# Performance work log

Hardware: AMD Instinct MI355X
Metric: run time of the kernel (lower is better)

## Reference

```python
import jax, jax.numpy as jnp
import numpy as np

B, C, H, W = 64, 3, 32, 32
HID, PRE, VMAX = 128, 32, 256
IN_DIM = C * 5 - 1  # 14


def setup_inputs() -> dict:
    key = jax.random.key(0)
    ks = jax.random.split(key, 9)
    s = 0.05
    return {
        "x": jax.random.uniform(ks[0], (B, C, H, W), dtype=jnp.float32),
        "W_pre": jax.random.normal(ks[1], (PRE, IN_DIM), dtype=jnp.float32) * s,
        "b_pre": jnp.zeros((PRE,), dtype=jnp.float32),
        "W_ih": jax.random.normal(ks[2], (3 * HID, PRE), dtype=jnp.float32) * s,
        "b_ih": jnp.zeros((3 * HID,), dtype=jnp.float32),
        "W_hh": jax.random.normal(ks[3], (3 * HID, HID), dtype=jnp.float32) * s,
        "b_hh": jnp.zeros((3 * HID,), dtype=jnp.float32),
        "W_post": jax.random.normal(ks[4], (VMAX, HID), dtype=jnp.float32) * s,
        "b_post": jnp.zeros((VMAX,), dtype=jnp.float32),
    }


def _img2input(x):
    # x: [b, c, h, w] -> [b, (h-2)*(w-2)*c, 5c-1], matching torch _img2input
    b, c, h, w = x.shape
    xp = jnp.transpose(x, (0, 2, 3, 1))  # [b,h,w,c]
    tl = xp[:, :-2, :-2, :]
    tc = xp[:, :-2, 1:-1, :]
    tr = xp[:, :-2, 2:, :]
    lf = xp[:, 1:-1, :-2, :]
    ct = xp[:, 1:-1, 1:-1, :]
    base = jnp.concatenate([tl, tc, tr, lf], axis=-1)  # [b,h-2,w-2,4c]
    base = jnp.broadcast_to(base[..., None, :], base.shape[:3] + (c, 4 * c))
    # tail[ic, ic1] = center[ic1] if ic1 < ic else -1
    mask = jnp.arange(c - 1)[None, :] < jnp.arange(c)[:, None]  # [c, c-1]
    tail = jnp.where(mask, ct[..., None, :c - 1], -1.0)  # [b,h-2,w-2,c,c-1]
    y = jnp.concatenate([base, tail], axis=-1)  # [b,h-2,w-2,c,5c-1]
    return y.reshape(b, (h - 2) * (w - 2) * c, 5 * c - 1)


def reference(x, W_pre, b_pre, W_ih, b_ih, W_hh, b_hh, W_post, b_post):
    b, c, h, w = x.shape
    inp = _img2input(x)                                   # [b, T, 5c-1]
    pre = jax.nn.sigmoid(inp @ W_pre.T + b_pre)           # [b, T, PRE]
    xg = pre @ W_ih.T + b_ih                              # [b, T, 3*HID]
    xg_t = jnp.transpose(xg, (1, 0, 2))                   # [T, b, 3*HID]

    def step(h_prev, xt):
        hg = h_prev @ W_hh.T + b_hh
        xr, xz, xn = jnp.split(xt, 3, axis=-1)
        hr, hz, hn = jnp.split(hg, 3, axis=-1)
        r = jax.nn.sigmoid(xr + hr)
        z = jax.nn.sigmoid(xz + hz)
        n = jnp.tanh(xn + r * hn)
        h_new = (1.0 - z) * n + z * h_prev
        return h_new, h_new

    h0 = jnp.zeros((b, W_hh.shape[1]), dtype=x.dtype)
    _, hs = jax.lax.scan(step, h0, xg_t)                  # [T, b, HID]
    hs = jnp.transpose(hs, (1, 0, 2))                     # [b, T, HID]
    out = hs @ W_post.T + b_post                          # [b, T, VMAX]
    vmax = W_post.shape[0]
    out = out.reshape(b, h - 2, w - 2, c, vmax)
    out = jnp.transpose(out, (0, 3, 1, 2, 4))             # [b, c, h-2, w-2, vmax]
    out = jnp.pad(out, ((0, 0), (0, 0), (1, 1), (1, 1), (0, 0)))
    return out  # [b, c, h, w, vmax]
```

## Files before the change

kernel.cpp:

```cpp
#include <hip/hip_runtime.h>
#include <cstdint>

#define B_    64
#define T_    2700
#define HID_  128
#define PRE_  32
#define VMAX_ 256
#define NG_   16
#define NB_   4
#define TCH_  27
#define TSZ_  100

typedef _Float16 half2_t __attribute__((ext_vector_type(2)));
typedef _Float16 half4_t __attribute__((ext_vector_type(4)));
typedef _Float16 half8_t __attribute__((ext_vector_type(8)));
typedef float    f32x4_t __attribute__((ext_vector_type(4)));
union H8u { half8_t v; half2_t p[4]; };

#define MFMA32(A, Bv, C) __builtin_amdgcn_mfma_f32_16x16x32_f16((A), (Bv), (C), 0, 0, 0)

#if __has_builtin(__builtin_amdgcn_fdot2)
__device__ __forceinline__ float FDOT2(half2_t a, half2_t b, float c) {
    return __builtin_amdgcn_fdot2(a, b, c, false);
}
#else
__device__ __forceinline__ float FDOT2(half2_t a, half2_t b, float c) {
    return c + (float)a[0] * (float)b[0] + (float)a[1] * (float)b[1];
}
#endif

__device__ __forceinline__ half2_t mk2(float a, float b) {
    half2_t r; r[0] = (_Float16)a; r[1] = (_Float16)b; return r;
}
__device__ __forceinline__ float fast_sigmoid(float x) {
    float t = __builtin_amdgcn_exp2f(-1.4426950408889634f * x);
    return __builtin_amdgcn_rcpf(1.0f + t);
}
__device__ __forceinline__ float fast_tanh(float x) {
    float t = __builtin_amdgcn_exp2f(2.885390081777927f * x);
    return 1.0f - 2.0f * __builtin_amdgcn_rcpf(t + 1.0f);
}
template<int CTRL>
__device__ __forceinline__ float dpp_add(float x) {
    int t = __builtin_amdgcn_update_dpp(0, __float_as_int(x), CTRL, 0xF, 0xF, true);
    return x + __int_as_float(t);
}
__device__ __forceinline__ void fma4(float4& a, const float4 w, const float4 h) {
    a.x += w.x * h.x; a.y += w.y * h.y; a.z += w.z * h.z; a.w += w.w * h.w;
}
__device__ __forceinline__ float hsum4(const float4 a) {
    return (a.x + a.y) + (a.z + a.w);
}
__device__ __forceinline__ float pick_reg(f32x4_t v, int addr, int sel) {
    float t0 = __int_as_float(__builtin_amdgcn_ds_bpermute(addr, __float_as_int(v[0])));
    float t1 = __int_as_float(__builtin_amdgcn_ds_bpermute(addr, __float_as_int(v[1])));
    float t2 = __int_as_float(__builtin_amdgcn_ds_bpermute(addr, __float_as_int(v[2])));
    float t3 = __int_as_float(__builtin_amdgcn_ds_bpermute(addr, __float_as_int(v[3])));
    float a = (sel & 1) ? t1 : t0;
    float b = (sel & 1) ? t3 : t2;
    return (sel & 2) ? b : a;
}

__global__ __launch_bounds__(256) void k_pre(const float* __restrict__ x,
                                             const float* __restrict__ W_pre,
                                             const float* __restrict__ b_pre,
                                             _Float16* __restrict__ pre16) {
    int tid  = blockIdx.x * 256 + threadIdx.x;
    int i    = tid & 31;
    int rest = tid >> 5;
    int c    = rest % 3;
    int r2   = rest / 3;
    int p    = r2 % 900;
    int b    = r2 / 900;
    int r    = p / 30;
    int cc   = p - r * 30;
    const float* xb = x + b * 3072 + r * 32 + cc;
    float f0 = xb[0],    f1  = xb[1024], f2  = xb[2048];
    float f3 = xb[1],    f4  = xb[1025], f5  = xb[2049];
    float f6 = xb[2],    f7  = xb[1026], f8  = xb[2050];
    float f9 = xb[32],   f10 = xb[1056], f11 = xb[2080];
    float ct0 = xb[33],  ct1 = xb[1057];
    float f12 = (c >= 1) ? ct0 : -1.0f;
    float f13 = (c >= 2) ? ct1 : -1.0f;
    const float* w = W_pre + i * 14;
    float d = b_pre[i];
    d += f0*w[0]  + f1*w[1]  + f2*w[2]  + f3*w[3]  + f4*w[4]  + f5*w[5]  + f6*w[6]
       + f7*w[7]  + f8*w[8]  + f9*w[9]  + f10*w[10] + f11*w[11] + f12*w[12] + f13*w[13];

    int t  = p * 3 + c;
    int g  = b >> 2;
    int cs = b & 3;
    size_t base = ((size_t)g * T_ + t) * 128;
    int idx = ((i >> 3) << 5) | (cs << 3) | (i & 7);
    pre16[base + idx] = (_Float16)fast_sigmoid(d);
}

template<bool FULL>
__global__ __launch_bounds__(512) void k_xg(const float* __restrict__ W_ih,
                                            const float* __restrict__ b_ih,
                                            const float* __restrict__ b_hh,
                                            const _Float16* __restrict__ pre16,
                                            _Float16* __restrict__ xg16) {
    const int tid = threadIdx.x;
    const int g   = blockIdx.x / TCH_;
    const int tc  = blockIdx.x % TCH_;
    const int u3  = (tid >> 6) * 16 + ((tid & 63) >> 2);
    const int c4  = tid & 3;

    half2_t wr[16], wz[16], wn[16];
    const float* Wn = W_ih + (size_t)(256 + u3) * PRE_;
#pragma unroll
    for (int k2 = 0; k2 < 16; ++k2) wn[k2] = mk2(Wn[2*k2], Wn[2*k2 + 1]);
    const float bn = b_ih[256 + u3];
    float br = 0.f, bz = 0.f;
    if (FULL) {
        const float* Wr = W_ih + (size_t)u3 * PRE_;
        const float* Wz = W_ih + (size_t)(128 + u3) * PRE_;
#pragma unroll
        for (int k2 = 0; k2 < 16; ++k2) {
            wr[k2] = mk2(Wr[2*k2], Wr[2*k2 + 1]);
            wz[k2] = mk2(Wz[2*k2], Wz[2*k2 + 1]);
        }
        br = b_ih[u3] + b_hh[u3];
        bz = b_ih[128 + u3] + b_hh[128 + u3];
    }

    const char* preg = (const char*)pre16 + ((size_t)g * T_ + (size_t)tc * TSZ_) * 256 + c4 * 16;
    H8u pc0, pc1, pc2, pc3;
    pc0.v = *(const half8_t*)(preg +   0);
    pc1.v = *(const half8_t*)(preg +  64);
    pc2.v = *(const half8_t*)(preg + 128);
    pc3.v = *(const half8_t*)(preg + 192);

    for (int tt = 0; tt < TSZ_; ++tt) {
        const int ttn = (tt + 1 < TSZ_) ? tt + 1 : tt;
        H8u n0, n1, n2, n3;
        n0.v = *(const half8_t*)(preg + (size_t)ttn * 256 +   0);
        n1.v = *(const half8_t*)(preg + (size_t)ttn * 256 +  64);
        n2.v = *(const half8_t*)(preg + (size_t)ttn * 256 + 128);
        n3.v = *(const half8_t*)(preg + (size_t)ttn * 256 + 192);

        float an = bn;
#pragma unroll
        for (int j2 = 0; j2 < 4; ++j2) an = FDOT2(wn[ 0 + j2], pc0.p[j2], an);
#pragma unroll
        for (int j2 = 0; j2 < 4; ++j2) an = FDOT2(wn[ 4 + j2], pc1.p[j2], an);
#pragma unroll
        for (int j2 = 0; j2 < 4; ++j2) an = FDOT2(wn[ 8 + j2], pc2.p[j2], an);
#pragma unroll
        for (int j2 = 0; j2 < 4; ++j2) an = FDOT2(wn[12 + j2], pc3.p[j2], an);

        const size_t t = (size_t)tc * TSZ_ + tt;
        if (FULL) {
            float ar = br, az = bz;
#pragma unroll
            for (int j2 = 0; j2 < 4; ++j2) { ar = FDOT2(wr[ 0 + j2], pc0.p[j2], ar); az = FDOT2(wz[ 0 + j2], pc0.p[j2], az); }
#pragma unroll
            for (int j2 = 0; j2 < 4; ++j2) { ar = FDOT2(wr[ 4 + j2], pc1.p[j2], ar); az = FDOT2(wz[ 4 + j2], pc1.p[j2], az); }
#pragma unroll
            for (int j2 = 0; j2 < 4; ++j2) { ar = FDOT2(wr[ 8 + j2], pc2.p[j2], ar); az = FDOT2(wz[ 8 + j2], pc2.p[j2], az); }
#pragma unroll
            for (int j2 = 0; j2 < 4; ++j2) { ar = FDOT2(wr[12 + j2], pc3.p[j2], ar); az = FDOT2(wz[12 + j2], pc3.p[j2], az); }
            half4_t o;
            o[0] = (_Float16)ar; o[1] = (_Float16)az; o[2] = (_Float16)an; o[3] = (_Float16)0.f;
            *(half4_t*)((char*)xg16 + (((size_t)g * T_ + t) * 512 + tid) * 8) = o;
        } else {
            xg16[((size_t)g * T_ + t) * 512 + tid] = (_Float16)an;
        }
        pc0 = n0; pc1 = n1; pc2 = n2; pc3 = n3;
    }
}

template<bool FULL>
__global__ __launch_bounds__(512, 1) void k_scan(const float* __restrict__ W_ih,
                                                 const float* __restrict__ b_ih,
                                                 const float* __restrict__ W_hh,
                                                 const float* __restrict__ b_hh,
                                                 const _Float16* __restrict__ pre16,
                                                 const _Float16* __restrict__ xg16,
                                                 _Float16* __restrict__ hs16) {
    __shared__ __align__(16) _Float16 hbuf[2][4][4][4][8];

    const int tid  = threadIdx.x;
    const int g    = blockIdx.x;
    const int w    = tid >> 6;
    const int lane = tid & 63;
    const int lo   = lane & 15;
    const int hi   = lane >> 4;
    const int c4   = lane & 3;
    const int row  = w * 16 + lo;

    half8_t Ar[5], Az[5], Ahn[4];
#pragma unroll
    for (int kc = 0; kc < 4; ++kc) {
        half8_t ar, az, an;
#pragma unroll
        for (int j = 0; j < 8; ++j) {
            int k = kc * 32 + hi * 8 + j;
            ar[j] = (_Float16)W_hh[row * HID_ + k];
            az[j] = (_Float16)W_hh[(128 + row) * HID_ + k];
            an[j] = (_Float16)W_hh[(256 + row) * HID_ + k];
        }
        Ar[kc] = ar; Az[kc] = az; Ahn[kc] = an;
    }
    if (!FULL) {
        half8_t ar, az;
#pragma unroll
        for (int j = 0; j < 8; ++j) {
            int k = hi * 8 + j;
            ar[j] = (_Float16)W_ih[row * PRE_ + k];
            az[j] = (_Float16)W_ih[(128 + row) * PRE_ + k];
        }
        Ar[4] = ar; Az[4] = az;
    }

    const int u3 = w * 16 + (lane >> 2);
    float br = 0.f, bz = 0.f;
    if (!FULL) { br = b_ih[u3] + b_hh[u3]; bz = b_ih[128 + u3] + b_hh[128 + u3]; }
    const float bhn = b_hh[256 + u3];
    const int srcaddr = ((((lane >> 4) << 4) | c4) << 2);
    const int sel     = (lane >> 2) & 3;

    const char* preg  = (const char*)pre16 + (size_t)g * T_ * 256;
    const int   pfoff = hi * 64 + c4 * 16;
    const char*      xgp = (const char*)xg16 + (((size_t)g * T_) * 512 + tid) * 8;
    const _Float16*  xgs = xg16 + (size_t)g * T_ * 512 + tid;
    _Float16* hsb = hs16 + (size_t)(g * NB_ + c4) * T_ * HID_ + u3;

    const int kc_w = u3 >> 5;
    const int hi_w = (u3 >> 3) & 3;
    const int j_w  = u3 & 7;

    ((uint32_t*)hbuf)[tid] = 0u;

    half8_t  pf{};
    half4_t  xh{};
    _Float16 xnf = (_Float16)0.f;
    if (FULL) xh = *(const half4_t*)xgp;
    else { pf = *(const half8_t*)(preg + pfoff); xnf = xgs[0]; }
    float hprev = 0.0f;
    __syncthreads();

    for (int t = 0; t < T_; ++t) {
        const int tn = (t + 1 < T_) ? (t + 1) : t;
        half8_t pfn{}; half4_t xhn{}; _Float16 xnn = (_Float16)0.f;
        if (FULL) {
            xhn = *(const half4_t*)(xgp + (size_t)tn * 4096);
        } else {
            pfn = *(const half8_t*)(preg + (size_t)tn * 256 + pfoff);
            xnn = xgs[(size_t)tn * 512];
        }

        const int rb = t & 1;
        half8_t hB[4];
#pragma unroll
        for (int kc = 0; kc < 4; ++kc)
            hB[kc] = *(const half8_t*)&hbuf[rb][kc][hi][c4][0];

        const f32x4_t Z4 = {0.f, 0.f, 0.f, 0.f};
        f32x4_t r = Z4, z = Z4, n = Z4;
        r = MFMA32(Ar[0],  hB[0], r);
        z = MFMA32(Az[0],  hB[0], z);
        n = MFMA32(Ahn[0], hB[0], n);
        r = MFMA32(Ar[1],  hB[1], r);
        z = MFMA32(Az[1],  hB[1], z);
        n = MFMA32(Ahn[1], hB[1], n);
        r = MFMA32(Ar[2],  hB[2], r);
        z = MFMA32(Az[2],  hB[2], z);
        n = MFMA32(Ahn[2], hB[2], n);
        r = MFMA32(Ar[3],  hB[3], r);
        z = MFMA32(Az[3],  hB[3], z);
        n = MFMA32(Ahn[3], hB[3], n);
        if (!FULL) {
            r = MFMA32(Ar[4], pf, r);
            z = MFMA32(Az[4], pf, z);
        }

        float srr = pick_reg(r, srcaddr, sel);
        float szz = pick_reg(z, srcaddr, sel);
        float shn = pick_reg(n, srcaddr, sel) + bhn;
        float sxn;
        if (FULL) { srr += (float)xh[0]; szz += (float)xh[1]; sxn = (float)xh[2]; }
        else      { srr += br;           szz += bz;           sxn = (float)xnf;  }

        float rg   = fast_sigmoid(srr);
        float zg   = fast_sigmoid(szz);
        float ng   = fast_tanh(sxn + rg * shn);
        float hnew = ng + zg * (hprev - ng);
        hprev = hnew;
        _Float16 h16 = (_Float16)hnew;

        hbuf[rb ^ 1][kc_w][hi_w][c4][j_w] = h16;
        hsb[(size_t)t * HID_] = h16;

        if (FULL) xh = xhn; else { pf = pfn; xnf = xnn; }

        asm volatile("s_waitcnt lgkmcnt(0)" ::: "memory");
        __builtin_amdgcn_s_barrier();
    }
}

__global__ __launch_bounds__(512, 4) void k_post(const float* __restrict__ W_post,
                                                 const float* __restrict__ b_post,
                                                 const _Float16* __restrict__ hs,
                                                 float* __restrict__ out) {
    __shared__ __align__(16) float sh[2][HID_];
    const int tid  = threadIdx.x;
    const int v    = tid >> 1;
    const int hf   = tid & 1;
    const int blk  = blockIdx.x;
    const int i    = blk & 31;
    const int rest = blk >> 5;
    const int ch   = rest % 3;
    const int b    = rest / 3;
    float* outb = out + ((size_t)(b * 3 + ch) * 1024 + i * 32) * VMAX_;

    if (i == 0 || i == 31) {
        if (hf == 0) {
#pragma unroll
            for (int jc = 0; jc < 32; ++jc) outb[jc * VMAX_ + v] = 0.0f;
        }
        return;
    }

    float4 wp[16];
    const float4* wpp = (const float4*)(W_post + (size_t)v * HID_ + hf * 64);
#pragma unroll
    for (int k = 0; k < 16; ++k) wp[k] = wpp[k];
    const float bp = b_post[v];

    const _Float16* hsb = hs + (size_t)b * T_ * HID_;
    const int trow = (i - 1) * 30;

    if (tid < 32) {
        half4_t hv = ((const half4_t*)(hsb + (size_t)(trow * 3 + ch) * HID_))[tid];
        float4 f = {(float)hv[0], (float)hv[1], (float)hv[2], (float)hv[3]};
        ((float4*)sh[1])[tid] = f;
    }
    if (hf == 0) { outb[v] = 0.0f; outb[31 * VMAX_ + v] = 0.0f; }
    __syncthreads();

    for (int jc = 1; jc <= 30; ++jc) {
        if (tid < 32 && jc < 30) {
            half4_t hv = ((const half4_t*)(hsb + (size_t)((trow + jc) * 3 + ch) * HID_))[tid];
            float4 f = {(float)hv[0], (float)hv[1], (float)hv[2], (float)hv[3]};
            ((float4*)sh[(jc + 1) & 1])[tid] = f;
        }
        const float4* h4 = (const float4*)sh[jc & 1] + hf * 16;
        float4 a0 = {0,0,0,0}, a1 = {0,0,0,0}, a2 = {0,0,0,0}, a3 = {0,0,0,0};
#pragma unroll
        for (int k = 0; k < 16; k += 4) {
            fma4(a0, wp[k],     h4[k]);
            fma4(a1, wp[k + 1], h4[k + 1]);
            fma4(a2, wp[k + 2], h4[k + 2]);
            fma4(a3, wp[k + 3], h4[k + 3]);
        }
        float s = (hsum4(a0) + hsum4(a1)) + (hsum4(a2) + hsum4(a3));
        s = dpp_add<0xB1>(s);
        if (hf == 0) outb[jc * VMAX_ + v] = bp + s;
        __syncthreads();
    }
}

extern "C" void kernel_launch(void* const* d_in, const int* in_sizes, int n_in,
                              void* d_out, int out_size, void* d_ws, size_t ws_size,
                              hipStream_t stream) {
    const float* x      = (const float*)d_in[0];
    const float* W_pre  = (const float*)d_in[1];
    const float* b_pre  = (const float*)d_in[2];
    const float* W_ih   = (const float*)d_in[3];
    const float* b_ih   = (const float*)d_in[4];
    const float* W_hh   = (const float*)d_in[5];
    const float* b_hh   = (const float*)d_in[6];
    const float* W_post = (const float*)d_in[7];
    const float* b_post = (const float*)d_in[8];
    float* out = (float*)d_out;

    const size_t pre_bytes = (size_t)NG_ * T_ * 256;
    const size_t xg_full   = (size_t)NG_ * T_ * 512 * 8;
    const size_t xg_fb     = (size_t)NG_ * T_ * 512 * 2;
    const size_t hs_bytes  = (size_t)B_ * T_ * HID_ * 2;
    const bool full = ws_size >= pre_bytes + xg_full + hs_bytes;

    _Float16* pre16 = (_Float16*)d_ws;
    _Float16* xg    = (_Float16*)((char*)d_ws + pre_bytes);
    _Float16* hs16  = (_Float16*)((char*)d_ws + pre_bytes + (full ? xg_full : xg_fb));

    k_pre<<<21600, 256, 0, stream>>>(x, W_pre, b_pre, pre16);
    if (full) {
        k_xg<true><<<NG_ * TCH_, 512, 0, stream>>>(W_ih, b_ih, b_hh, pre16, xg);
        k_scan<true><<<NG_, 512, 0, stream>>>(W_ih, b_ih, W_hh, b_hh, pre16, xg, hs16);
    } else {
        k_xg<false><<<NG_ * TCH_, 512, 0, stream>>>(W_ih, b_ih, b_hh, pre16, xg);
        k_scan<false><<<NG_, 512, 0, stream>>>(W_ih, b_ih, W_hh, b_hh, pre16, xg, hs16);
    }
    k_post<<<6144, 512, 0, stream>>>(W_post, b_post, hs16, out);
}
```

Before: 2.102 ms.

## Remap full-path scan so active lanes compute four hidden units per step

The full-workspace path of the GRU scan is split into its own kernel. Gate results are now read straight from the MFMA accumulator registers, so a quarter of the lanes each handle four hidden units. This drops the cross-lane pick_reg shuffles and lets each of those lanes issue one vectorized half4 store to LDS and to the hidden-state output. The xg producer layout is permuted to match, and the time loop is unrolled by two with prefetch two steps ahead. The risk is that three quarters of the lanes sit idle during the gate math, which lengthens the per-step serial activation work on the critical path.

```diff
diff --git a/kernel.cpp b/kernel.cpp
--- a/kernel.cpp
+++ b/kernel.cpp
@@ -95,35 +95,30 @@
     pre16[base + idx] = (_Float16)fast_sigmoid(d);
 }
 
-template<bool FULL>
-__global__ __launch_bounds__(512) void k_xg(const float* __restrict__ W_ih,
-                                            const float* __restrict__ b_ih,
-                                            const float* __restrict__ b_hh,
-                                            const _Float16* __restrict__ pre16,
-                                            _Float16* __restrict__ xg16) {
+__global__ __launch_bounds__(512) void k_xg_full(const float* __restrict__ W_ih,
+                                                 const float* __restrict__ b_ih,
+                                                 const float* __restrict__ b_hh,
+                                                 const _Float16* __restrict__ pre16,
+                                                 _Float16* __restrict__ xg16) {
     const int tid = threadIdx.x;
     const int g   = blockIdx.x / TCH_;
     const int tc  = blockIdx.x % TCH_;
-    const int u3  = (tid >> 6) * 16 + ((tid & 63) >> 2);
-    const int c4  = tid & 3;
+    const int u3  = ((tid >> 6) << 4) | (((tid >> 4) & 3) << 2) | (tid & 3);
+    const int c4  = (tid >> 2) & 3;
 
     half2_t wr[16], wz[16], wn[16];
+    const float* Wr = W_ih + (size_t)u3 * PRE_;
+    const float* Wz = W_ih + (size_t)(128 + u3) * PRE_;
     const float* Wn = W_ih + (size_t)(256 + u3) * PRE_;
 #pragma unroll
-    for (int k2 = 0; k2 < 16; ++k2) wn[k2] = mk2(Wn[2*k2], Wn[2*k2 + 1]);
+    for (int k2 = 0; k2 < 16; ++k2) {
+        wr[k2] = mk2(Wr[2*k2], Wr[2*k2 + 1]);
+        wz[k2] = mk2(Wz[2*k2], Wz[2*k2 + 1]);
+        wn[k2] = mk2(Wn[2*k2], Wn[2*k2 + 1]);
+    }
+    const float br = b_ih[u3] + b_hh[u3];
+    const float bz = b_ih[128 + u3] + b_hh[128 + u3];
     const float bn = b_ih[256 + u3];
-    float br = 0.f, bz = 0.f;
-    if (FULL) {
-        const float* Wr = W_ih + (size_t)u3 * PRE_;
-        const float* Wz = W_ih + (size_t)(128 + u3) * PRE_;
-#pragma unroll
-        for (int k2 = 0; k2 < 16; ++k2) {
-            wr[k2] = mk2(Wr[2*k2], Wr[2*k2 + 1]);
-            wz[k2] = mk2(Wz[2*k2], Wz[2*k2 + 1]);
-        }
-        br = b_ih[u3] + b_hh[u3];
-        bz = b_ih[128 + u3] + b_hh[128 + u3];
-    }
 
     const char* preg = (const char*)pre16 + ((size_t)g * T_ + (size_t)tc * TSZ_) * 256 + c4 * 16;
     H8u pc0, pc1, pc2, pc3;
@@ -140,45 +135,65 @@
         n2.v = *(const half8_t*)(preg + (size_t)ttn * 256 + 128);
         n3.v = *(const half8_t*)(preg + (size_t)ttn * 256 + 192);
 
+        float ar = br, az = bz, an = bn;
+#pragma unroll
+        for (int j2 = 0; j2 < 4; ++j2) { ar = FDOT2(wr[ 0+j2], pc0.p[j2], ar); az = FDOT2(wz[ 0+j2], pc0.p[j2], az); an = FDOT2(wn[ 0+j2], pc0.p[j2], an); }
+#pragma unroll
+        for (int j2 = 0; j2 < 4; ++j2) { ar = FDOT2(wr[ 4+j2], pc1.p[j2], ar); az = FDOT2(wz[ 4+j2], pc1.p[j2], az); an = FDOT2(wn[ 4+j2], pc1.p[j2], an); }
+#pragma unroll
+        for (int j2 = 0; j2 < 4; ++j2) { ar = FDOT2(wr[ 8+j2], pc2.p[j2], ar); az = FDOT2(wz[ 8+j2], pc2.p[j2], az); an = FDOT2(wn[ 8+j2], pc2.p[j2], an); }
+#pragma unroll
+        for (int j2 = 0; j2 < 4; ++j2) { ar = FDOT2(wr[12+j2], pc3.p[j2], ar); az = FDOT2(wz[12+j2], pc3.p[j2], az); an = FDOT2(wn[12+j2], pc3.p[j2], an); }
+
+        const size_t t = (size_t)tc * TSZ_ + tt;
+        half4_t o;
+        o[0] = (_Float16)ar; o[1] = (_Float16)az; o[2] = (_Float16)an; o[3] = (_Float16)0.f;
+        *(half4_t*)((char*)xg16 + (((size_t)g * T_ + t) * 512 + tid) * 8) = o;
+        pc0 = n0; pc1 = n1; pc2 = n2; pc3 = n3;
+    }
+}
+
+__global__ __launch_bounds__(512) void k_xg_fb(const float* __restrict__ W_ih,
+                                               const float* __restrict__ b_ih,
+                                               const _Float16* __restrict__ pre16,
+                                               _Float16* __restrict__ xg16) {
+    const int tid = threadIdx.x;
+    const int g   = blockIdx.x / TCH_;
+    const int tc  = blockIdx.x % TCH_;
+    const int u3  = (tid >> 6) * 16 + ((tid & 63) >> 2);
+    const int c4  = tid & 3;
+
+    half2_t wn[16];
+    const float* Wn = W_ih + (size_t)(256 + u3) * PRE_;
+#pragma unroll
+    for (int k2 = 0; k2 < 16; ++k2) wn[k2] = mk2(Wn[2*k2], Wn[2*k2 + 1]);
+    const float bn = b_ih[256 + u3];
+
+    const char* preg = (const char*)pre16 + ((size_t)g * T_ + (size_t)tc * TSZ_) * 256 + c4 * 16;
+    for (int tt = 0; tt < TSZ_; ++tt) {
+        H8u pc0, pc1, pc2, pc3;
+        pc0.v = *(const half8_t*)(preg + (size_t)tt * 256 +   0);
+        pc1.v = *(const half8_t*)(preg + (size_t)tt * 256 +  64);
+        pc2.v = *(const half8_t*)(preg + (size_t)tt * 256 + 128);
+        pc3.v = *(const half8_t*)(preg + (size_t)tt * 256 + 192);
         float an = bn;
 #pragma unroll
-        for (int j2 = 0; j2 < 4; ++j2) an = FDOT2(wn[ 0 + j2], pc0.p[j2], an);
-#pragma unroll
-        for (int j2 = 0; j2 < 4; ++j2) an = FDOT2(wn[ 4 + j2], pc1.p[j2], an);
-#pragma unroll
-        for (int j2 = 0; j2 < 4; ++j2) an = FDOT2(wn[ 8 + j2], pc2.p[j2], an);
-#pragma unroll
-        for (int j2 = 0; j2 < 4; ++j2) an = FDOT2(wn[12 + j2], pc3.p[j2], an);
-
+        for (int j2 = 0; j2 < 4; ++j2) an = FDOT2(wn[ 0+j2], pc0.p[j2], an);
+#pragma unroll
+        for (int j2 = 0; j2 < 4; ++j2) an = FDOT2(wn[ 4+j2], pc1.p[j2], an);
+#pragma unroll
+        for (int j2 = 0; j2 < 4; ++j2) an = FDOT2(wn[ 8+j2], pc2.p[j2], an);
+#pragma unroll
+        for (int j2 = 0; j2 < 4; ++j2) an = FDOT2(wn[12+j2], pc3.p[j2], an);
         const size_t t = (size_t)tc * TSZ_ + tt;
-        if (FULL) {
-            float ar = br, az = bz;
-#pragma unroll
-            for (int j2 = 0; j2 < 4; ++j2) { ar = FDOT2(wr[ 0 + j2], pc0.p[j2], ar); az = FDOT2(wz[ 0 + j2], pc0.p[j2], az); }
-#pragma unroll
-            for (int j2 = 0; j2 < 4; ++j2) { ar = FDOT2(wr[ 4 + j2], pc1.p[j2], ar); az = FDOT2(wz[ 4 + j2], pc1.p[j2], az); }
-#pragma unroll
-            for (int j2 = 0; j2 < 4; ++j2) { ar = FDOT2(wr[ 8 + j2], pc2.p[j2], ar); az = FDOT2(wz[ 8 + j2], pc2.p[j2], az); }
-#pragma unroll
-            for (int j2 = 0; j2 < 4; ++j2) { ar = FDOT2(wr[12 + j2], pc3.p[j2], ar); az = FDOT2(wz[12 + j2], pc3.p[j2], az); }
-            half4_t o;
-            o[0] = (_Float16)ar; o[1] = (_Float16)az; o[2] = (_Float16)an; o[3] = (_Float16)0.f;
-            *(half4_t*)((char*)xg16 + (((size_t)g * T_ + t) * 512 + tid) * 8) = o;
-        } else {
-            xg16[((size_t)g * T_ + t) * 512 + tid] = (_Float16)an;
-        }
-        pc0 = n0; pc1 = n1; pc2 = n2; pc3 = n3;
-    }
-}
-
-template<bool FULL>
-__global__ __launch_bounds__(512, 1) void k_scan(const float* __restrict__ W_ih,
-                                                 const float* __restrict__ b_ih,
-                                                 const float* __restrict__ W_hh,
-                                                 const float* __restrict__ b_hh,
-                                                 const _Float16* __restrict__ pre16,
-                                                 const _Float16* __restrict__ xg16,
-                                                 _Float16* __restrict__ hs16) {
+        xg16[((size_t)g * T_ + t) * 512 + tid] = (_Float16)an;
+    }
+}
+
+__global__ __launch_bounds__(512, 1) void k_scan_full(const float* __restrict__ W_hh,
+                                                      const float* __restrict__ b_hh,
+                                                      const _Float16* __restrict__ xg16,
+                                                      _Float16* __restrict__ hs16) {
     __shared__ __align__(16) _Float16 hbuf[2][4][4][4][8];
 
     const int tid  = threadIdx.x;
@@ -190,7 +205,7 @@
     const int c4   = lane & 3;
     const int row  = w * 16 + lo;
 
-    half8_t Ar[5], Az[5], Ahn[4];
+    half8_t Ar[4], Az[4], Ahn[4];
 #pragma unroll
     for (int kc = 0; kc < 4; ++kc) {
         half8_t ar, az, an;
@@ -203,7 +218,104 @@
         }
         Ar[kc] = ar; Az[kc] = az; Ahn[kc] = an;
     }
-    if (!FULL) {
+
+    const bool act = (lo < 4);
+    const int u0 = w * 16 + hi * 4;
+    const f32x4_t bhn4 = *(const f32x4_t*)(b_hh + 256 + u0);
+
+    const char* xgp = (const char*)xg16 + (size_t)g * T_ * 4096
+                    + (size_t)(((w << 4) | (hi << 2) | c4) << 5);
+    _Float16* hsb = hs16 + (size_t)(g * NB_ + c4) * T_ * HID_ + u0;
+
+    const int kc_w  = u0 >> 5;
+    const int hi2_w = (u0 >> 3) & 3;
+    const int j0_w  = u0 & 7;
+
+    ((uint32_t*)hbuf)[tid] = 0u;
+
+    half8_t xA0 = *(const half8_t*)(xgp);
+    half8_t xA1 = *(const half8_t*)(xgp + 16);
+    half8_t xB0 = *(const half8_t*)(xgp + 4096);
+    half8_t xB1 = *(const half8_t*)(xgp + 4096 + 16);
+    f32x4_t hp = {0.f, 0.f, 0.f, 0.f};
+    __syncthreads();
+
+#define SCAN_STEP(RB, X0, X1, TT)                                              \
+    {                                                                          \
+        half8_t hB0 = *(const half8_t*)&hbuf[RB][0][hi][c4][0];                \
+        half8_t hB1 = *(const half8_t*)&hbuf[RB][1][hi][c4][0];                \
+        half8_t hB2 = *(const half8_t*)&hbuf[RB][2][hi][c4][0];                \
+        half8_t hB3 = *(const half8_t*)&hbuf[RB][3][hi][c4][0];                \
+        f32x4_t r = {0.f,0.f,0.f,0.f}, z = {0.f,0.f,0.f,0.f}, n = {0.f,0.f,0.f,0.f}; \
+        r = MFMA32(Ar[0], hB0, r); z = MFMA32(Az[0], hB0, z); n = MFMA32(Ahn[0], hB0, n); \
+        r = MFMA32(Ar[1], hB1, r); z = MFMA32(Az[1], hB1, z); n = MFMA32(Ahn[1], hB1, n); \
+        r = MFMA32(Ar[2], hB2, r); z = MFMA32(Az[2], hB2, z); n = MFMA32(Ahn[2], hB2, n); \
+        r = MFMA32(Ar[3], hB3, r); z = MFMA32(Az[3], hB3, z); n = MFMA32(Ahn[3], hB3, n); \
+        if (act) {                                                             \
+            half4_t hq;                                                        \
+            _Pragma("unroll")                                                  \
+            for (int q = 0; q < 4; ++q) {                                      \
+                half8_t xv = (q < 2) ? (X0) : (X1);                            \
+                const int o = (q & 1) * 4;                                     \
+                float rg = fast_sigmoid(r[q] + (float)xv[o]);                  \
+                float zg = fast_sigmoid(z[q] + (float)xv[o + 1]);              \
+                float ng = fast_tanh((float)xv[o + 2] + rg * (n[q] + bhn4[q])); \
+                float hv = ng + zg * (hp[q] - ng);                             \
+                hp[q] = hv;                                                    \
+                hq[q] = (_Float16)hv;                                          \
+            }                                                                  \
+            *(half4_t*)&hbuf[(RB) ^ 1][kc_w][hi2_w][c4][j0_w] = hq;            \
+            *(half4_t*)(hsb + (size_t)(TT) * HID_) = hq;                       \
+        }                                                                      \
+        asm volatile("s_waitcnt lgkmcnt(0)" ::: "memory");                     \
+        __builtin_amdgcn_s_barrier();                                          \
+    }
+
+    for (int t = 0; t < T_; t += 2) {
+        const size_t o2 = (size_t)((t + 2 < T_) ? t + 2 : T_ - 1) * 4096;
+        const size_t o3 = (size_t)((t + 3 < T_) ? t + 3 : T_ - 1) * 4096;
+        half8_t xC0 = *(const half8_t*)(xgp + o2);
+        half8_t xC1 = *(const half8_t*)(xgp + o2 + 16);
+        SCAN_STEP(0, xA0, xA1, t);
+        half8_t xD0 = *(const half8_t*)(xgp + o3);
+        half8_t xD1 = *(const half8_t*)(xgp + o3 + 16);
+        SCAN_STEP(1, xB0, xB1, t + 1);
+        xA0 = xC0; xA1 = xC1; xB0 = xD0; xB1 = xD1;
+    }
+#undef SCAN_STEP
+}
+
+__global__ __launch_bounds__(512, 1) void k_scan_fb(const float* __restrict__ W_ih,
+                                                    const float* __restrict__ b_ih,
+                                                    const float* __restrict__ W_hh,
+                                                    const float* __restrict__ b_hh,
+                                                    const _Float16* __restrict__ pre16,
+                                                    const _Float16* __restrict__ xg16,
+                                                    _Float16* __restrict__ hs16) {
+    __shared__ __align__(16) _Float16 hbuf[2][4][4][4][8];
+    const int tid  = threadIdx.x;
+    const int g    = blockIdx.x;
+    const int w    = tid >> 6;
+    const int lane = tid & 63;
+    const int lo   = lane & 15;
+    const int hi   = lane >> 4;
+    const int c4   = lane & 3;
+    const int row  = w * 16 + lo;
+
+    half8_t Ar[5], Az[5], Ahn[4];
+#pragma unroll
+    for (int kc = 0; kc < 4; ++kc) {
+        half8_t ar, az, an;
+#pragma unroll
+        for (int j = 0; j < 8; ++j) {
+            int k = kc * 32 + hi * 8 + j;
+            ar[j] = (_Float16)W_hh[row * HID_ + k];
+            az[j] = (_Float16)W_hh[(128 + row) * HID_ + k];
+            an[j] = (_Float16)W_hh[(256 + row) * HID_ + k];
+        }
+        Ar[kc] = ar; Az[kc] = az; Ahn[kc] = an;
+    }
+    {
         half8_t ar, az;
 #pragma unroll
         for (int j = 0; j < 8; ++j) {
@@ -215,16 +327,15 @@
     }
 
     const int u3 = w * 16 + (lane >> 2);
-    float br = 0.f, bz = 0.f;
-    if (!FULL) { br = b_ih[u3] + b_hh[u3]; bz = b_ih[128 + u3] + b_hh[128 + u3]; }
+    const float br  = b_ih[u3] + b_hh[u3];
+    const float bz  = b_ih[128 + u3] + b_hh[128 + u3];
     const float bhn = b_hh[256 + u3];
     const int srcaddr = ((((lane >> 4) << 4) | c4) << 2);
     const int sel     = (lane >> 2) & 3;
 
     const char* preg  = (const char*)pre16 + (size_t)g * T_ * 256;
     const int   pfoff = hi * 64 + c4 * 16;
-    const char*      xgp = (const char*)xg16 + (((size_t)g * T_) * 512 + tid) * 8;
-    const _Float16*  xgs = xg16 + (size_t)g * T_ * 512 + tid;
+    const _Float16* xgs = xg16 + (size_t)g * T_ * 512 + tid;
     _Float16* hsb = hs16 + (size_t)(g * NB_ + c4) * T_ * HID_ + u3;
 
     const int kc_w = u3 >> 5;
@@ -233,23 +344,15 @@
 
     ((uint32_t*)hbuf)[tid] = 0u;
 
-    half8_t  pf{};
-    half4_t  xh{};
-    _Float16 xnf = (_Float16)0.f;
-    if (FULL) xh = *(const half4_t*)xgp;
-    else { pf = *(const half8_t*)(preg + pfoff); xnf = xgs[0]; }
+    half8_t pf = *(const half8_t*)(preg + pfoff);
+    _Float16 xnf = xgs[0];
     float hprev = 0.0f;
     __syncthreads();
 
     for (int t = 0; t < T_; ++t) {
         const int tn = (t + 1 < T_) ? (t + 1) : t;
-        half8_t pfn{}; half4_t xhn{}; _Float16 xnn = (_Float16)0.f;
-        if (FULL) {
-            xhn = *(const half4_t*)(xgp + (size_t)tn * 4096);
-        } else {
-            pfn = *(const half8_t*)(preg + (size_t)tn * 256 + pfoff);
-            xnn = xgs[(size_t)tn * 512];
-        }
+        half8_t pfn = *(const half8_t*)(preg + (size_t)tn * 256 + pfoff);
+        _Float16 xnn = xgs[(size_t)tn * 512];
 
         const int rb = t & 1;
         half8_t hB[4];
@@ -271,17 +374,13 @@
         r = MFMA32(Ar[3],  hB[3], r);
         z = MFMA32(Az[3],  hB[3], z);
         n = MFMA32(Ahn[3], hB[3], n);
-        if (!FULL) {
-            r = MFMA32(Ar[4], pf, r);
-            z = MFMA32(Az[4], pf, z);
-        }
-
-        float srr = pick_reg(r, srcaddr, sel);
-        float szz = pick_reg(z, srcaddr, sel);
+        r = MFMA32(Ar[4], pf, r);
+        z = MFMA32(Az[4], pf, z);
+
+        float srr = pick_reg(r, srcaddr, sel) + br;
+        float szz = pick_reg(z, srcaddr, sel) + bz;
         float shn = pick_reg(n, srcaddr, sel) + bhn;
-        float sxn;
-        if (FULL) { srr += (float)xh[0]; szz += (float)xh[1]; sxn = (float)xh[2]; }
-        else      { srr += br;           szz += bz;           sxn = (float)xnf;  }
+        float sxn = (float)xnf;
 
         float rg   = fast_sigmoid(srr);
         float zg   = fast_sigmoid(szz);
@@ -293,8 +392,7 @@
         hbuf[rb ^ 1][kc_w][hi_w][c4][j_w] = h16;
         hsb[(size_t)t * HID_] = h16;
 
-        if (FULL) xh = xhn; else { pf = pfn; xnf = xnn; }
-
+        pf = pfn; xnf = xnn;
         asm volatile("s_waitcnt lgkmcnt(0)" ::: "memory");
         __builtin_amdgcn_s_barrier();
     }
@@ -388,11 +486,11 @@
 
     k_pre<<<21600, 256, 0, stream>>>(x, W_pre, b_pre, pre16);
     if (full) {
-        k_xg<true><<<NG_ * TCH_, 512, 0, stream>>>(W_ih, b_ih, b_hh, pre16, xg);
-        k_scan<true><<<NG_, 512, 0, stream>>>(W_ih, b_ih, W_hh, b_hh, pre16, xg, hs16);
+        k_xg_full<<<NG_ * TCH_, 512, 0, stream>>>(W_ih, b_ih, b_hh, pre16, xg);
+        k_scan_full<<<NG_, 512, 0, stream>>>(W_hh, b_hh, xg, hs16);
     } else {
-        k_xg<false><<<NG_ * TCH_, 512, 0, stream>>>(W_ih, b_ih, b_hh, pre16, xg);
-        k_scan<false><<<NG_, 512, 0, stream>>>(W_ih, b_ih, W_hh, b_hh, pre16, xg, hs16);
+        k_xg_fb<<<NG_ * TCH_, 512, 0, stream>>>(W_ih, b_ih, pre16, xg);
+        k_scan_fb<<<NG_, 512, 0, stream>>>(W_ih, b_ih, W_hh, b_hh, pre16, xg, hs16);
     }
     k_post<<<6144, 512, 0, stream>>>(W_post, b_post, hs16, out);
 }
```

Measured after the change: 2.444 ms. +16.3%, slower.

## Use MFMA for output projection, drop fallback path, unroll scan by two

Applied to the files above, without the earlier changes.

Rewrites k_post so each block computes its 30x256 output tile with fp16 16x16x32 MFMA on a converted fp16 W_post, replacing the per-thread float FMA loop with its 30 barriers. A new k_wcvt kernel converts W_post into the workspace, reusing the pre16 region once k_xg is done with it. The scan loop is unrolled by two so the xg prefetches for steps t+2 and t+3 are issued earlier. The small-workspace fallback is removed and the full xg buffer is always assumed, which fails if the workspace is too small. fp16 W_post adds rounding error.

```diff
diff --git a/kernel.cpp b/kernel.cpp
--- a/kernel.cpp
+++ b/kernel.cpp
@@ -39,17 +39,6 @@
 __device__ __forceinline__ float fast_tanh(float x) {
     float t = __builtin_amdgcn_exp2f(2.885390081777927f * x);
     return 1.0f - 2.0f * __builtin_amdgcn_rcpf(t + 1.0f);
-}
-template<int CTRL>
-__device__ __forceinline__ float dpp_add(float x) {
-    int t = __builtin_amdgcn_update_dpp(0, __float_as_int(x), CTRL, 0xF, 0xF, true);
-    return x + __int_as_float(t);
-}
-__device__ __forceinline__ void fma4(float4& a, const float4 w, const float4 h) {
-    a.x += w.x * h.x; a.y += w.y * h.y; a.z += w.z * h.z; a.w += w.w * h.w;
-}
-__device__ __forceinline__ float hsum4(const float4 a) {
-    return (a.x + a.y) + (a.z + a.w);
 }
 __device__ __forceinline__ float pick_reg(f32x4_t v, int addr, int sel) {
     float t0 = __int_as_float(__builtin_amdgcn_ds_bpermute(addr, __float_as_int(v[0])));
@@ -95,7 +84,6 @@
     pre16[base + idx] = (_Float16)fast_sigmoid(d);
 }
 
-template<bool FULL>
 __global__ __launch_bounds__(512) void k_xg(const float* __restrict__ W_ih,
                                             const float* __restrict__ b_ih,
                                             const float* __restrict__ b_hh,
@@ -108,22 +96,18 @@
     const int c4  = tid & 3;
 
     half2_t wr[16], wz[16], wn[16];
+    const float* Wr = W_ih + (size_t)u3 * PRE_;
+    const float* Wz = W_ih + (size_t)(128 + u3) * PRE_;
     const float* Wn = W_ih + (size_t)(256 + u3) * PRE_;
 #pragma unroll
-    for (int k2 = 0; k2 < 16; ++k2) wn[k2] = mk2(Wn[2*k2], Wn[2*k2 + 1]);
+    for (int k2 = 0; k2 < 16; ++k2) {
+        wr[k2] = mk2(Wr[2*k2], Wr[2*k2 + 1]);
+        wz[k2] = mk2(Wz[2*k2], Wz[2*k2 + 1]);
+        wn[k2] = mk2(Wn[2*k2], Wn[2*k2 + 1]);
+    }
+    const float br = b_ih[u3] + b_hh[u3];
+    const float bz = b_ih[128 + u3] + b_hh[128 + u3];
     const float bn = b_ih[256 + u3];
-    float br = 0.f, bz = 0.f;
-    if (FULL) {
-        const float* Wr = W_ih + (size_t)u3 * PRE_;
-        const float* Wz = W_ih + (size_t)(128 + u3) * PRE_;
-#pragma unroll
-        for (int k2 = 0; k2 < 16; ++k2) {
-            wr[k2] = mk2(Wr[2*k2], Wr[2*k2 + 1]);
-            wz[k2] = mk2(Wz[2*k2], Wz[2*k2 + 1]);
-        }
-        br = b_ih[u3] + b_hh[u3];
-        bz = b_ih[128 + u3] + b_hh[128 + u3];
-    }
 
     const char* preg = (const char*)pre16 + ((size_t)g * T_ + (size_t)tc * TSZ_) * 256 + c4 * 16;
     H8u pc0, pc1, pc2, pc3;
@@ -140,43 +124,32 @@
         n2.v = *(const half8_t*)(preg + (size_t)ttn * 256 + 128);
         n3.v = *(const half8_t*)(preg + (size_t)ttn * 256 + 192);
 
-        float an = bn;
-#pragma unroll
-        for (int j2 = 0; j2 < 4; ++j2) an = FDOT2(wn[ 0 + j2], pc0.p[j2], an);
-#pragma unroll
-        for (int j2 = 0; j2 < 4; ++j2) an = FDOT2(wn[ 4 + j2], pc1.p[j2], an);
-#pragma unroll
-        for (int j2 = 0; j2 < 4; ++j2) an = FDOT2(wn[ 8 + j2], pc2.p[j2], an);
-#pragma unroll
-        for (int j2 = 0; j2 < 4; ++j2) an = FDOT2(wn[12 + j2], pc3.p[j2], an);
+        float ar = br, az = bz, an = bn;
+#pragma unroll
+        for (int j2 = 0; j2 < 4; ++j2) { ar = FDOT2(wr[ 0+j2], pc0.p[j2], ar); az = FDOT2(wz[ 0+j2], pc0.p[j2], az); an = FDOT2(wn[ 0+j2], pc0.p[j2], an); }
+#pragma unroll
+        for (int j2 = 0; j2 < 4; ++j2) { ar = FDOT2(wr[ 4+j2], pc1.p[j2], ar); az = FDOT2(wz[ 4+j2], pc1.p[j2], az); an = FDOT2(wn[ 4+j2], pc1.p[j2], an); }
+#pragma unroll
+        for (int j2 = 0; j2 < 4; ++j2) { ar = FDOT2(wr[ 8+j2], pc2.p[j2], ar); az = FDOT2(wz[ 8+j2], pc2.p[j2], az); an = FDOT2(wn[ 8+j2], pc2.p[j2], an); }
+#pragma unroll
+        for (int j2 = 0; j2 < 4; ++j2) { ar = FDOT2(wr[12+j2], pc3.p[j2], ar); az = FDOT2(wz[12+j2], pc3.p[j2], az); an = FDOT2(wn[12+j2], pc3.p[j2], an); }
 
         const size_t t = (size_t)tc * TSZ_ + tt;
-        if (FULL) {
-            float ar = br, az = bz;
-#pragma unroll
-            for (int j2 = 0; j2 < 4; ++j2) { ar = FDOT2(wr[ 0 + j2], pc0.p[j2], ar); az = FDOT2(wz[ 0 + j2], pc0.p[j2], az); }
-#pragma unroll
-            for (int j2 = 0; j2 < 4; ++j2) { ar = FDOT2(wr[ 4 + j2], pc1.p[j2], ar); az = FDOT2(wz[ 4 + j2], pc1.p[j2], az); }
-#pragma unroll
-            for (int j2 = 0; j2 < 4; ++j2) { ar = FDOT2(wr[ 8 + j2], pc2.p[j2], ar); az = FDOT2(wz[ 8 + j2], pc2.p[j2], az); }
-#pragma unroll
-            for (int j2 = 0; j2 < 4; ++j2) { ar = FDOT2(wr[12 + j2], pc3.p[j2], ar); az = FDOT2(wz[12 + j2], pc3.p[j2], az); }
-            half4_t o;
-            o[0] = (_Float16)ar; o[1] = (_Float16)az; o[2] = (_Float16)an; o[3] = (_Float16)0.f;
-            *(half4_t*)((char*)xg16 + (((size_t)g * T_ + t) * 512 + tid) * 8) = o;
-        } else {
-            xg16[((size_t)g * T_ + t) * 512 + tid] = (_Float16)an;
-        }
+        half4_t o;
+        o[0] = (_Float16)ar; o[1] = (_Float16)az; o[2] = (_Float16)an; o[3] = (_Float16)0.f;
+        *(half4_t*)((char*)xg16 + (((size_t)g * T_ + t) * 512 + tid) * 8) = o;
         pc0 = n0; pc1 = n1; pc2 = n2; pc3 = n3;
     }
 }
 
-template<bool FULL>
-__global__ __launch_bounds__(512, 1) void k_scan(const float* __restrict__ W_ih,
-                                                 const float* __restrict__ b_ih,
-                                                 const float* __restrict__ W_hh,
+__global__ __launch_bounds__(256) void k_wcvt(const float* __restrict__ W_post,
+                                              _Float16* __restrict__ w16) {
+    int idx = blockIdx.x * 256 + threadIdx.x;
+    w16[idx] = (_Float16)W_post[idx];
+}
+
+__global__ __launch_bounds__(512, 1) void k_scan(const float* __restrict__ W_hh,
                                                  const float* __restrict__ b_hh,
-                                                 const _Float16* __restrict__ pre16,
                                                  const _Float16* __restrict__ xg16,
                                                  _Float16* __restrict__ hs16) {
     __shared__ __align__(16) _Float16 hbuf[2][4][4][4][8];
@@ -190,7 +163,7 @@
     const int c4   = lane & 3;
     const int row  = w * 16 + lo;
 
-    half8_t Ar[5], Az[5], Ahn[4];
+    half8_t Ar[4], Az[4], Ahn[4];
 #pragma unroll
     for (int kc = 0; kc < 4; ++kc) {
         half8_t ar, az, an;
@@ -203,28 +176,13 @@
         }
         Ar[kc] = ar; Az[kc] = az; Ahn[kc] = an;
     }
-    if (!FULL) {
-        half8_t ar, az;
-#pragma unroll
-        for (int j = 0; j < 8; ++j) {
-            int k = hi * 8 + j;
-            ar[j] = (_Float16)W_ih[row * PRE_ + k];
-            az[j] = (_Float16)W_ih[(128 + row) * PRE_ + k];
-        }
-        Ar[4] = ar; Az[4] = az;
-    }
 
     const int u3 = w * 16 + (lane >> 2);
-    float br = 0.f, bz = 0.f;
-    if (!FULL) { br = b_ih[u3] + b_hh[u3]; bz = b_ih[128 + u3] + b_hh[128 + u3]; }
     const float bhn = b_hh[256 + u3];
     const int srcaddr = ((((lane >> 4) << 4) | c4) << 2);
     const int sel     = (lane >> 2) & 3;
 
-    const char* preg  = (const char*)pre16 + (size_t)g * T_ * 256;
-    const int   pfoff = hi * 64 + c4 * 16;
-    const char*      xgp = (const char*)xg16 + (((size_t)g * T_) * 512 + tid) * 8;
-    const _Float16*  xgs = xg16 + (size_t)g * T_ * 512 + tid;
+    const char* xgp = (const char*)xg16 + ((size_t)g * T_ * 512 + tid) * 8;
     _Float16* hsb = hs16 + (size_t)(g * NB_ + c4) * T_ * HID_ + u3;
 
     const int kc_w = u3 >> 5;
@@ -233,81 +191,55 @@
 
     ((uint32_t*)hbuf)[tid] = 0u;
 
-    half8_t  pf{};
-    half4_t  xh{};
-    _Float16 xnf = (_Float16)0.f;
-    if (FULL) xh = *(const half4_t*)xgp;
-    else { pf = *(const half8_t*)(preg + pfoff); xnf = xgs[0]; }
+    half4_t xA = *(const half4_t*)(xgp);
+    half4_t xB = *(const half4_t*)(xgp + 4096);
     float hprev = 0.0f;
     __syncthreads();
 
-    for (int t = 0; t < T_; ++t) {
-        const int tn = (t + 1 < T_) ? (t + 1) : t;
-        half8_t pfn{}; half4_t xhn{}; _Float16 xnn = (_Float16)0.f;
-        if (FULL) {
-            xhn = *(const half4_t*)(xgp + (size_t)tn * 4096);
-        } else {
-            pfn = *(const half8_t*)(preg + (size_t)tn * 256 + pfoff);
-            xnn = xgs[(size_t)tn * 512];
-        }
-
-        const int rb = t & 1;
-        half8_t hB[4];
-#pragma unroll
-        for (int kc = 0; kc < 4; ++kc)
-            hB[kc] = *(const half8_t*)&hbuf[rb][kc][hi][c4][0];
-
-        const f32x4_t Z4 = {0.f, 0.f, 0.f, 0.f};
-        f32x4_t r = Z4, z = Z4, n = Z4;
-        r = MFMA32(Ar[0],  hB[0], r);
-        z = MFMA32(Az[0],  hB[0], z);
-        n = MFMA32(Ahn[0], hB[0], n);
-        r = MFMA32(Ar[1],  hB[1], r);
-        z = MFMA32(Az[1],  hB[1], z);
-        n = MFMA32(Ahn[1], hB[1], n);
-        r = MFMA32(Ar[2],  hB[2], r);
-        z = MFMA32(Az[2],  hB[2], z);
-        n = MFMA32(Ahn[2], hB[2], n);
-        r = MFMA32(Ar[3],  hB[3], r);
-        z = MFMA32(Az[3],  hB[3], z);
-        n = MFMA32(Ahn[3], hB[3], n);
-        if (!FULL) {
-            r = MFMA32(Ar[4], pf, r);
-            z = MFMA32(Az[4], pf, z);
-        }
-
-        float srr = pick_reg(r, srcaddr, sel);
-        float szz = pick_reg(z, srcaddr, sel);
-        float shn = pick_reg(n, srcaddr, sel) + bhn;
-        float sxn;
-        if (FULL) { srr += (float)xh[0]; szz += (float)xh[1]; sxn = (float)xh[2]; }
-        else      { srr += br;           szz += bz;           sxn = (float)xnf;  }
-
-        float rg   = fast_sigmoid(srr);
-        float zg   = fast_sigmoid(szz);
-        float ng   = fast_tanh(sxn + rg * shn);
-        float hnew = ng + zg * (hprev - ng);
-        hprev = hnew;
-        _Float16 h16 = (_Float16)hnew;
-
-        hbuf[rb ^ 1][kc_w][hi_w][c4][j_w] = h16;
-        hsb[(size_t)t * HID_] = h16;
-
-        if (FULL) xh = xhn; else { pf = pfn; xnf = xnn; }
-
-        asm volatile("s_waitcnt lgkmcnt(0)" ::: "memory");
-        __builtin_amdgcn_s_barrier();
-    }
-}
-
-__global__ __launch_bounds__(512, 4) void k_post(const float* __restrict__ W_post,
+#define SCAN_STEP(RB, X, TT)                                                   \
+    {                                                                          \
+        half8_t hB0 = *(const half8_t*)&hbuf[RB][0][hi][c4][0];                \
+        half8_t hB1 = *(const half8_t*)&hbuf[RB][1][hi][c4][0];                \
+        half8_t hB2 = *(const half8_t*)&hbuf[RB][2][hi][c4][0];                \
+        half8_t hB3 = *(const half8_t*)&hbuf[RB][3][hi][c4][0];                \
+        f32x4_t r = {0.f,0.f,0.f,0.f}, z = {0.f,0.f,0.f,0.f}, n = {0.f,0.f,0.f,0.f}; \
+        r = MFMA32(Ar[0], hB0, r); z = MFMA32(Az[0], hB0, z); n = MFMA32(Ahn[0], hB0, n); \
+        r = MFMA32(Ar[1], hB1, r); z = MFMA32(Az[1], hB1, z); n = MFMA32(Ahn[1], hB1, n); \
+        r = MFMA32(Ar[2], hB2, r); z = MFMA32(Az[2], hB2, z); n = MFMA32(Ahn[2], hB2, n); \
+        r = MFMA32(Ar[3], hB3, r); z = MFMA32(Az[3], hB3, z); n = MFMA32(Ahn[3], hB3, n); \
+        float srr = pick_reg(r, srcaddr, sel) + (float)(X)[0];                 \
+        float szz = pick_reg(z, srcaddr, sel) + (float)(X)[1];                 \
+        float shn = pick_reg(n, srcaddr, sel) + bhn;                           \
+        float sxn = (float)(X)[2];                                             \
+        float rg   = fast_sigmoid(srr);                                        \
+        float zg   = fast_sigmoid(szz);                                        \
+        float ng   = fast_tanh(sxn + rg * shn);                                \
+        float hnew = ng + zg * (hprev - ng);                                   \
+        hprev = hnew;                                                          \
+        _Float16 h16 = (_Float16)hnew;                                         \
+        hbuf[(RB) ^ 1][kc_w][hi_w][c4][j_w] = h16;                             \
+        hsb[(size_t)(TT) * HID_] = h16;                                        \
+        asm volatile("s_waitcnt lgkmcnt(0)" ::: "memory");                     \
+        __builtin_amdgcn_s_barrier();                                          \
+    }
+
+    for (int t = 0; t < T_; t += 2) {
+        const size_t o2 = (size_t)((t + 2 < T_) ? t + 2 : T_ - 1) * 4096;
+        const size_t o3 = (size_t)((t + 3 < T_) ? t + 3 : T_ - 1) * 4096;
+        half4_t xC = *(const half4_t*)(xgp + o2);
+        SCAN_STEP(0, xA, t);
+        half4_t xD = *(const half4_t*)(xgp + o3);
+        SCAN_STEP(1, xB, t + 1);
+        xA = xC; xB = xD;
+    }
+#undef SCAN_STEP
+}
+
+__global__ __launch_bounds__(512, 2) void k_post(const _Float16* __restrict__ w16,
                                                  const float* __restrict__ b_post,
                                                  const _Float16* __restrict__ hs,
                                                  float* __restrict__ out) {
-    __shared__ __align__(16) float sh[2][HID_];
     const int tid  = threadIdx.x;
-    const int v    = tid >> 1;
-    const int hf   = tid & 1;
     const int blk  = blockIdx.x;
     const int i    = blk & 31;
     const int rest = blk >> 5;
@@ -315,50 +247,62 @@
     const int b    = rest / 3;
     float* outb = out + ((size_t)(b * 3 + ch) * 1024 + i * 32) * VMAX_;
 
+    const float4 z4 = {0.f, 0.f, 0.f, 0.f};
     if (i == 0 || i == 31) {
-        if (hf == 0) {
-#pragma unroll
-            for (int jc = 0; jc < 32; ++jc) outb[jc * VMAX_ + v] = 0.0f;
+        float4* o4 = (float4*)outb;
+#pragma unroll
+        for (int k = 0; k < 4; ++k) o4[k * 512 + tid] = z4;
+        return;
+    }
+    if (tid < 64)       ((float4*)outb)[tid] = z4;
+    else if (tid < 128) ((float4*)(outb + 31 * VMAX_))[tid - 64] = z4;
+
+    const int wv   = tid >> 6;
+    const int lane = tid & 63;
+    const int lo   = lane & 15;
+    const int hi   = lane >> 4;
+    const int t0   = (i - 1) * 90 + ch;
+    const _Float16* hsb = hs + (size_t)b * T_ * HID_;
+
+    half8_t Af[2][4], Bf[2][4];
+#pragma unroll
+    for (int mt = 0; mt < 2; ++mt) {
+        int m = mt * 16 + lo; if (m > 29) m = 29;
+        const _Float16* ap = hsb + (size_t)(t0 + 3 * m) * HID_ + hi * 8;
+#pragma unroll
+        for (int kc = 0; kc < 4; ++kc) Af[mt][kc] = *(const half8_t*)(ap + kc * 32);
+    }
+    const int vb = wv * 32;
+#pragma unroll
+    for (int nt = 0; nt < 2; ++nt) {
+        const _Float16* bp = w16 + (size_t)(vb + nt * 16 + lo) * HID_ + hi * 8;
+#pragma unroll
+        for (int kc = 0; kc < 4; ++kc) Bf[nt][kc] = *(const half8_t*)(bp + kc * 32);
+    }
+    const float bp0 = b_post[vb + lo];
+    const float bp1 = b_post[vb + 16 + lo];
+
+    f32x4_t a00 = {0.f,0.f,0.f,0.f}, a01 = a00, a10 = a00, a11 = a00;
+#pragma unroll
+    for (int kc = 0; kc < 4; ++kc) {
+        a00 = MFMA32(Af[0][kc], Bf[0][kc], a00);
+        a01 = MFMA32(Af[0][kc], Bf[1][kc], a01);
+        a10 = MFMA32(Af[1][kc], Bf[0][kc], a10);
+        a11 = MFMA32(Af[1][kc], Bf[1][kc], a11);
+    }
+
+#pragma unroll
+    for (int q = 0; q < 4; ++q) {
+        {
+            float* orow = outb + (size_t)(1 + 4 * hi + q) * VMAX_;
+            orow[vb + lo]      = a00[q] + bp0;
+            orow[vb + 16 + lo] = a01[q] + bp1;
         }
-        return;
-    }
-
-    float4 wp[16];
-    const float4* wpp = (const float4*)(W_post + (size_t)v * HID_ + hf * 64);
-#pragma unroll
-    for (int k = 0; k < 16; ++k) wp[k] = wpp[k];
-    const float bp = b_post[v];
-
-    const _Float16* hsb = hs + (size_t)b * T_ * HID_;
-    const int trow = (i - 1) * 30;
-
-    if (tid < 32) {
-        half4_t hv = ((const half4_t*)(hsb + (size_t)(trow * 3 + ch) * HID_))[tid];
-        float4 f = {(float)hv[0], (float)hv[1], (float)hv[2], (float)hv[3]};
-        ((float4*)sh[1])[tid] = f;
-    }
-    if (hf == 0) { outb[v] = 0.0f; outb[31 * VMAX_ + v] = 0.0f; }
-    __syncthreads();
-
-    for (int jc = 1; jc <= 30; ++jc) {
-        if (tid < 32 && jc < 30) {
-            half4_t hv = ((const half4_t*)(hsb + (size_t)((trow + jc) * 3 + ch) * HID_))[tid];
-            float4 f = {(float)hv[0], (float)hv[1], (float)hv[2], (float)hv[3]};
-            ((float4*)sh[(jc + 1) & 1])[tid] = f;
+        if (4 * hi + q <= 13) {
+            float* orow = outb + (size_t)(17 + 4 * hi + q) * VMAX_;
+            orow[vb + lo]      = a10[q] + bp0;
+            orow[vb + 16 + lo] = a11[q] + bp1;
         }
-        const float4* h4 = (const float4*)sh[jc & 1] + hf * 16;
-        float4 a0 = {0,0,0,0}, a1 = {0,0,0,0}, a2 = {0,0,0,0}, a3 = {0,0,0,0};
-#pragma unroll
-        for (int k = 0; k < 16; k += 4) {
-            fma4(a0, wp[k],     h4[k]);
-            fma4(a1, wp[k + 1], h4[k + 1]);
-            fma4(a2, wp[k + 2], h4[k + 2]);
-            fma4(a3, wp[k + 3], h4[k + 3]);
-        }
-        float s = (hsum4(a0) + hsum4(a1)) + (hsum4(a2) + hsum4(a3));
-        s = dpp_add<0xB1>(s);
-        if (hf == 0) outb[jc * VMAX_ + v] = bp + s;
-        __syncthreads();
     }
 }
 
@@ -377,22 +321,15 @@
     float* out = (float*)d_out;
 
     const size_t pre_bytes = (size_t)NG_ * T_ * 256;
-    const size_t xg_full   = (size_t)NG_ * T_ * 512 * 8;
-    const size_t xg_fb     = (size_t)NG_ * T_ * 512 * 2;
-    const size_t hs_bytes  = (size_t)B_ * T_ * HID_ * 2;
-    const bool full = ws_size >= pre_bytes + xg_full + hs_bytes;
-
+    const size_t xg_bytes  = (size_t)NG_ * T_ * 512 * 8;
     _Float16* pre16 = (_Float16*)d_ws;
+    _Float16* w16   = (_Float16*)d_ws;
     _Float16* xg    = (_Float16*)((char*)d_ws + pre_bytes);
-    _Float16* hs16  = (_Float16*)((char*)d_ws + pre_bytes + (full ? xg_full : xg_fb));
-
-    k_pre<<<21600, 256, 0, stream>>>(x, W_pre, b_pre, pre16);
-    if (full) {
-        k_xg<true><<<NG_ * TCH_, 512, 0, stream>>>(W_ih, b_ih, b_hh, pre16, xg);
-        k_scan<true><<<NG_, 512, 0, stream>>>(W_ih, b_ih, W_hh, b_hh, pre16, xg, hs16);
-    } else {
-        k_xg<false><<<NG_ * TCH_, 512, 0, stream>>>(W_ih, b_ih, b_hh, pre16, xg);
-        k_scan<false><<<NG_, 512, 0, stream>>>(W_ih, b_ih, W_hh, b_hh, pre16, xg, hs16);
-    }
-    k_post<<<6144, 512, 0, stream>>>(W_post, b_post, hs16, out);
-}
+    _Float16* hs16  = (_Float16*)((char*)d_ws + pre_bytes + xg_bytes);
+
+    k_pre <<<21600, 256, 0, stream>>>(x, W_pre, b_pre, pre16);
+    k_xg  <<<NG_ * TCH_, 512, 0, stream>>>(W_ih, b_ih, b_hh, pre16, xg);
+    k_wcvt<<<128, 256, 0, stream>>>(W_post, w16);
+    k_scan<<<NG_, 512, 0, stream>>>(W_hh, b_hh, xg, hs16);
+    k_post<<<6144, 512, 0, stream>>>(w16, b_post, hs16, out);
+}
```

Result: no change. 2.118 ms (+0.8%).
